# Performance work log

Measured on AMD Instinct MI355X. Metric: run time of the kernel, lower is better.

The kernel has to match this reference:

```python
import jax, jax.numpy as jnp
import numpy as np

DIM = 128
CODEBOOK_SIZE = 1024
DECAY = 0.99
EPSILON = 1e-06


def setup_inputs() -> dict:
    key = jax.random.key(0)
    k1, k2, k3, k4 = jax.random.split(key, 4)
    x = jax.random.normal(k1, (64, 1024, DIM), dtype=jnp.float32)
    embed = jax.random.normal(k2, (CODEBOOK_SIZE, DIM), dtype=jnp.float32)
    # keep all codes above the dead-code threshold (2) so expire_codes_ is a no-op
    cluster_size = jax.random.uniform(k3, (CODEBOOK_SIZE,), dtype=jnp.float32) * 10.0 + 2.0
    embed_avg = jax.random.normal(k4, (CODEBOOK_SIZE, DIM), dtype=jnp.float32)
    return {"x": x, "embed": embed, "cluster_size": cluster_size, "embed_avg": embed_avg}


def reference(x, embed, cluster_size, embed_avg):
    shape = x.shape
    xf = x.reshape(-1, shape[-1])  # [N, D]

    # quantize: squared euclidean distances [N, K] then argmin
    dist = (
        jnp.sum(xf * xf, axis=1, keepdims=True)
        - 2.0 * (xf @ embed.T)
        + jnp.sum(embed * embed, axis=1)[None, :]
    )
    embed_ind_flat = jnp.argmin(dist, axis=-1)  # [N]
    embed_ind = embed_ind_flat.reshape(shape[:-1])

    # dequantize
    quantize = embed[embed_ind]  # [..., D]

    # training EMA updates (one-hot scatter accumulation)
    one_hot_sum = jax.ops.segment_sum(
        jnp.ones_like(embed_ind_flat, dtype=x.dtype), embed_ind_flat,
        num_segments=CODEBOOK_SIZE)
    embed_sum = jax.ops.segment_sum(xf, embed_ind_flat, num_segments=CODEBOOK_SIZE)  # [K, D]

    cluster_size_new = cluster_size * DECAY + one_hot_sum * (1.0 - DECAY)
    embed_avg_new = embed_avg * DECAY + embed_sum * (1.0 - DECAY)

    total = jnp.sum(cluster_size_new)
    smoothed = (cluster_size_new + EPSILON) / (total + EPSILON * CODEBOOK_SIZE) * total
    embed_new = embed_avg_new / smoothed[:, None]

    return quantize, embed_ind, cluster_size_new, embed_avg_new, embed_new
```

## Files before the change

kernel.cpp:

```cpp
#include <hip/hip_runtime.h>
#include <float.h>

#define DIMD   128
#define KCODES 1024
#define NROWS  65536
#define TAU    0.05f
#define SEG_R  8

typedef __attribute__((ext_vector_type(8)))  short short8;
typedef __attribute__((ext_vector_type(16))) float f32x16;

union U8 { uint4 u; short8 s; };

__device__ __forceinline__ unsigned bfr(float f) {
    unsigned u = __float_as_uint(f);
    return (u + 0x7fffu + ((u >> 16) & 1u)) >> 16;
}

__global__ void enorm_kernel(const float* __restrict__ embed, float* __restrict__ enorm) {
    int k = blockIdx.x * blockDim.x + threadIdx.x;
    if (k < KCODES) {
        const float4* e = (const float4*)(embed + (size_t)k * DIMD);
        float s = 0.f;
#pragma unroll
        for (int c = 0; c < DIMD / 4; ++c) {
            float4 v = e[c];
            s += v.x * v.x + v.y * v.y + v.z * v.z + v.w * v.w;
        }
        enorm[k] = s;
    }
}

__global__ __launch_bounds__(256) void preconvert_kernel(
    const float* __restrict__ embed, uint4* __restrict__ ehg, uint4* __restrict__ elg)
{
    int t = blockIdx.x * 256 + threadIdx.x;
    int chunk = t >> 9;
    int s = (t >> 6) & 7;
    int L = t & 63;
    const float* src = embed + ((size_t)(chunk * 32 + (L & 31)) * DIMD) + s * 16 + (L >> 5) * 8;
    float4 a = *(const float4*)src;
    float4 b = *(const float4*)(src + 4);
    float f[8] = {a.x, a.y, a.z, a.w, b.x, b.y, b.z, b.w};
    unsigned hi[8], lo[8];
#pragma unroll
    for (int j = 0; j < 8; ++j) {
        hi[j] = bfr(f[j]);
        float hf = __uint_as_float(hi[j] << 16);
        lo[j] = bfr(f[j] - hf);
    }
    uint4 H, Lw;
    H.x = hi[0] | (hi[1] << 16); H.y = hi[2] | (hi[3] << 16);
    H.z = hi[4] | (hi[5] << 16); H.w = hi[6] | (hi[7] << 16);
    Lw.x = lo[0] | (lo[1] << 16); Lw.y = lo[2] | (lo[3] << 16);
    Lw.z = lo[4] | (lo[5] << 16); Lw.w = lo[6] | (lo[7] << 16);
    ehg[t] = H;
    elg[t] = Lw;
}

__global__ __launch_bounds__(256, 2) void argmin_mfma(
    const float* __restrict__ x, const uint4* __restrict__ ehg, const uint4* __restrict__ elg,
    const float* __restrict__ enorm, int* __restrict__ ind_i, float* __restrict__ ind_f,
    int* __restrict__ wl, int* __restrict__ wl_cnt)
{
    __shared__ uint4 Bs[1024];

    const int tid  = threadIdx.x;
    const int wave = tid >> 6;
    const int lane = tid & 63;
    const int n    = lane & 31;
    const int h    = lane >> 5;
    const int row0 = blockIdx.x * 128;
    const int rowA = row0 + wave * 32 + n;

    uint4 xh[8], xl[8];
    const float* xrow = x + (size_t)rowA * DIMD + h * 8;
#pragma unroll
    for (int s = 0; s < 8; ++s) {
        float4 a = *(const float4*)(xrow + s * 16);
        float4 b = *(const float4*)(xrow + s * 16 + 4);
        float f[8] = {a.x, a.y, a.z, a.w, b.x, b.y, b.z, b.w};
        unsigned hi[8], lo[8];
#pragma unroll
        for (int j = 0; j < 8; ++j) {
            hi[j] = bfr(f[j]);
            float hf = __uint_as_float(hi[j] << 16);
            lo[j] = bfr(f[j] - hf);
        }
        xh[s].x = hi[0] | (hi[1] << 16); xh[s].y = hi[2] | (hi[3] << 16);
        xh[s].z = hi[4] | (hi[5] << 16); xh[s].w = hi[6] | (hi[7] << 16);
        xl[s].x = lo[0] | (lo[1] << 16); xl[s].y = lo[2] | (lo[3] << 16);
        xl[s].z = lo[4] | (lo[5] << 16); xl[s].w = lo[6] | (lo[7] << 16);
    }

    float bestv[16], best2[16];
    int   besti[16];
#pragma unroll
    for (int r = 0; r < 16; ++r) { bestv[r] = FLT_MAX; best2[r] = FLT_MAX; besti[r] = 0; }

    for (int chunk = 0; chunk < KCODES / 32; ++chunk) {
        __syncthreads();
        {
            const uint4* sh = ehg + chunk * 512;
            const uint4* sl = elg + chunk * 512;
#pragma unroll
            for (int i = 0; i < 2; ++i) {
                int idx = tid + i * 256;
                Bs[idx]       = sh[idx];
                Bs[512 + idx] = sl[idx];
            }
        }
        float ee_val = enorm[chunk * 32 + n];
        __syncthreads();

        f32x16 acc;
#pragma unroll
        for (int r = 0; r < 16; ++r) acc[r] = 0.f;

#pragma unroll
        for (int s = 0; s < 8; ++s) {
            U8 ah, al, bh, bl;
            ah.u = xh[s]; al.u = xl[s];
            bh.u = Bs[s * 64 + lane];
            bl.u = Bs[512 + s * 64 + lane];
            acc = __builtin_amdgcn_mfma_f32_32x32x16_bf16(ah.s, bh.s, acc, 0, 0, 0);
            acc = __builtin_amdgcn_mfma_f32_32x32x16_bf16(ah.s, bl.s, acc, 0, 0, 0);
            acc = __builtin_amdgcn_mfma_f32_32x32x16_bf16(al.s, bh.s, acc, 0, 0, 0);
        }

        const int nglob = chunk * 32 + n;
#pragma unroll
        for (int r = 0; r < 16; ++r) {
            float d = fmaf(-2.f, acc[r], ee_val);
            bool c1 = d < bestv[r];
            float t = c1 ? bestv[r] : d;
            best2[r] = fminf(best2[r], t);
            besti[r] = c1 ? nglob : besti[r];
            bestv[r] = fminf(bestv[r], d);
        }
    }

#pragma unroll
    for (int m = 1; m <= 16; m <<= 1) {
#pragma unroll
        for (int r = 0; r < 16; ++r) {
            float ov = __shfl_xor(bestv[r], m, 64);
            float o2 = __shfl_xor(best2[r], m, 64);
            int   oi = __shfl_xor(besti[r], m, 64);
            float hi = fmaxf(bestv[r], ov);
            best2[r] = fminf(fminf(best2[r], o2), hi);
            bool take = (ov < bestv[r]) || (ov == bestv[r] && oi < besti[r]);
            bestv[r] = take ? ov : bestv[r];
            besti[r] = take ? oi : besti[r];
        }
    }

    if (n == 0) {
#pragma unroll
        for (int r = 0; r < 16; ++r) {
            int row = row0 + wave * 32 + (r & 3) + 8 * (r >> 2) + 4 * h;
            ind_i[row] = besti[r];
            ind_f[row] = (float)besti[r];
            if (best2[r] - bestv[r] < TAU) {
                int p = atomicAdd(wl_cnt, 1);
                wl[p] = row;
            }
        }
    }
}

__global__ __launch_bounds__(256) void recheck_kernel(
    const float* __restrict__ x, const float* __restrict__ embed,
    const float* __restrict__ enorm, const int* __restrict__ wl,
    const int* __restrict__ wl_cnt, int* __restrict__ ind_i, float* __restrict__ ind_f)
{
    __shared__ float xs[DIMD];
    __shared__ float rv[256];
    __shared__ int   ri[256];
    const int tid = threadIdx.x;
    const int count = *wl_cnt;

    for (int i = blockIdx.x; i < count; i += gridDim.x) {
        const int row = wl[i];
        __syncthreads();
        if (tid < DIMD) xs[tid] = x[(size_t)row * DIMD + tid];
        __syncthreads();

        const float4* xs4 = (const float4*)xs;
        float xn = 0.f;
#pragma unroll 8
        for (int c = 0; c < 32; ++c) {
            float4 v = xs4[c];
            xn += v.x * v.x + v.y * v.y + v.z * v.z + v.w * v.w;
        }

        float bv = FLT_MAX; int bi = 0;
#pragma unroll
        for (int c = 0; c < 4; ++c) {
            int code = tid * 4 + c;
            const float4* er = (const float4*)(embed + (size_t)code * DIMD);
            float acc = 0.f;
#pragma unroll 8
            for (int kk = 0; kk < 32; ++kk) {
                float4 a = xs4[kk];
                float4 b = er[kk];
                acc += a.x * b.x + a.y * b.y + a.z * b.z + a.w * b.w;
            }
            float d = (xn - 2.0f * acc) + enorm[code];
            if (d < bv) { bv = d; bi = code; }
        }
        rv[tid] = bv; ri[tid] = bi;
        __syncthreads();
        for (int s = 128; s > 0; s >>= 1) {
            if (tid < s) {
                if (rv[tid + s] < rv[tid] || (rv[tid + s] == rv[tid] && ri[tid + s] < ri[tid])) {
                    rv[tid] = rv[tid + s]; ri[tid] = ri[tid + s];
                }
            }
            __syncthreads();
        }
        if (tid == 0) { ind_i[row] = ri[0]; ind_f[row] = (float)ri[0]; }
    }
}

__global__ __launch_bounds__(256) void hist_kernel(
    const int* __restrict__ ind, int* __restrict__ counts)
{
    __shared__ int h[KCODES];
    for (int i = threadIdx.x; i < KCODES; i += 256) h[i] = 0;
    __syncthreads();
    const int base = blockIdx.x * 2048;
    for (int i = threadIdx.x; i < 2048; i += 256) atomicAdd(&h[ind[base + i]], 1);
    __syncthreads();
    for (int i = threadIdx.x; i < KCODES; i += 256) {
        int v = h[i];
        if (v) atomicAdd(&counts[i], v);
    }
}

__global__ __launch_bounds__(1024) void scan_kernel(
    const int* __restrict__ counts, int* __restrict__ cursor)
{
    __shared__ int s[KCODES];
    const int t = threadIdx.x;
    int my = counts[t];
    s[t] = my;
    __syncthreads();
    for (int d = 1; d < KCODES; d <<= 1) {
        int v = (t >= d) ? s[t - d] : 0;
        __syncthreads();
        s[t] += v;
        __syncthreads();
    }
    cursor[t] = s[t] - my;
}

__global__ __launch_bounds__(256) void permgather_kernel(
    const float* __restrict__ embed, const int* __restrict__ ind,
    int* __restrict__ cursor, int* __restrict__ perm, int* __restrict__ codes,
    float* __restrict__ out_q)
{
    const int tid = threadIdx.x;
    const int row = blockIdx.x * 8 + (tid >> 5);
    const int c = tid & 31;
    const int k = ind[row];

    if (c == 0) {
        int pos = atomicAdd(&cursor[k], 1);
        perm[pos] = row;
        codes[pos] = k;
    }
    float4 e = *(const float4*)(embed + (size_t)k * DIMD + c * 4);
    *(float4*)(out_q + (size_t)row * DIMD + c * 4) = e;
}

__global__ __launch_bounds__(256) void segsum_kernel(
    const float* __restrict__ x, const int* __restrict__ perm,
    const int* __restrict__ codes, float* __restrict__ embed_sum)
{
    const int g = (blockIdx.x * 256 + threadIdx.x) >> 5;
    const int c = threadIdx.x & 31;
    const int base = g * SEG_R;

    float4 acc = {0.f, 0.f, 0.f, 0.f};
    int curk = codes[base];
#pragma unroll
    for (int j = 0; j < SEG_R; ++j) {
        int r = perm[base + j];
        int k = codes[base + j];
        float4 v = *(const float4*)(x + (size_t)r * DIMD + c * 4);
        if (k != curk) {
            float* dst = embed_sum + (size_t)curk * DIMD + c * 4;
            atomicAdd(dst + 0, acc.x);
            atomicAdd(dst + 1, acc.y);
            atomicAdd(dst + 2, acc.z);
            atomicAdd(dst + 3, acc.w);
            acc = v;
            curk = k;
        } else {
            acc.x += v.x; acc.y += v.y; acc.z += v.z; acc.w += v.w;
        }
    }
    float* dst = embed_sum + (size_t)curk * DIMD + c * 4;
    atomicAdd(dst + 0, acc.x);
    atomicAdd(dst + 1, acc.y);
    atomicAdd(dst + 2, acc.z);
    atomicAdd(dst + 3, acc.w);
}

__global__ __launch_bounds__(1024) void cluster_kernel(
    const float* __restrict__ cluster_size, const int* __restrict__ counts,
    float* __restrict__ out_cs, float* __restrict__ smoothed)
{
    __shared__ float red[1024];
    const int t = threadIdx.x;
    float cs = cluster_size[t] * 0.99f + (float)counts[t] * 0.01f;
    out_cs[t] = cs;
    red[t] = cs;
    __syncthreads();
    for (int s = 512; s > 0; s >>= 1) {
        if (t < s) red[t] += red[t + s];
        __syncthreads();
    }
    float total = red[0];
    smoothed[t] = (cs + 1e-6f) / (total + 1e-6f * (float)KCODES) * total;
}

__global__ void embed_kernel(
    const float* __restrict__ embed_avg, const float* __restrict__ embed_sum,
    const float* __restrict__ smoothed, float* __restrict__ out_ea,
    float* __restrict__ out_en)
{
    int i = blockIdx.x * blockDim.x + threadIdx.x;
    if (i < KCODES * DIMD) {
        float ea = embed_avg[i] * 0.99f + embed_sum[i] * 0.01f;
        out_ea[i] = ea;
        out_en[i] = ea / smoothed[i >> 7];
    }
}

extern "C" void kernel_launch(void* const* d_in, const int* in_sizes, int n_in,
                              void* d_out, int out_size, void* d_ws, size_t ws_size,
                              hipStream_t stream) {
    const float* x            = (const float*)d_in[0];
    const float* embed        = (const float*)d_in[1];
    const float* cluster_size = (const float*)d_in[2];
    const float* embed_avg    = (const float*)d_in[3];

    float* out     = (float*)d_out;
    float* out_q   = out;
    float* out_ind = out + 8388608;
    float* out_cs  = out + 8454144;
    float* out_ea  = out + 8455168;
    float* out_en  = out + 8586240;

    char* ws = (char*)d_ws;
    int*   ind_i     = (int*)(ws + 0);
    float* enorm     = (float*)(ws + 262144);
    int*   countsI   = (int*)(ws + 266240);
    int*   wl_cnt    = (int*)(ws + 270336);
    int*   cursor    = (int*)(ws + 274432);
    float* smoothed  = (float*)(ws + 278528);
    int*   perm      = (int*)(ws + 286720);
    int*   wl        = (int*)(ws + 548864);
    int*   codes     = (int*)(ws + 548864);
    uint4* ehg       = (uint4*)(ws + 811008);
    uint4* elg       = (uint4*)(ws + 1073152);
    float* embed_sum = (float*)(ws + 811008);

    hipMemsetAsync(countsI, 0, 8192, stream);

    enorm_kernel<<<4, 256, 0, stream>>>(embed, enorm);
    preconvert_kernel<<<64, 256, 0, stream>>>(embed, ehg, elg);
    argmin_mfma<<<NROWS / 128, 256, 0, stream>>>(x, ehg, elg, enorm, ind_i, out_ind, wl, wl_cnt);
    recheck_kernel<<<256, 256, 0, stream>>>(x, embed, enorm, wl, wl_cnt, ind_i, out_ind);
    hist_kernel<<<32, 256, 0, stream>>>(ind_i, countsI);
    scan_kernel<<<1, 1024, 0, stream>>>(countsI, cursor);
    hipMemsetAsync(embed_sum, 0, 524288, stream);
    permgather_kernel<<<NROWS / 8, 256, 0, stream>>>(embed, ind_i, cursor, perm, codes, out_q);
    segsum_kernel<<<(NROWS / SEG_R) * 32 / 256, 256, 0, stream>>>(x, perm, codes, embed_sum);
    cluster_kernel<<<1, 1024, 0, stream>>>(cluster_size, countsI, out_cs, smoothed);
    embed_kernel<<<(KCODES * DIMD + 255) / 256, 256, 0, stream>>>(
        embed_avg, embed_sum, smoothed, out_ea, out_en);
}
```

Baseline: 293.1 us.

## Fuse histogram and dequantize gather into argmin, merge prep and cluster kernels

The enorm and preconvert kernels are merged into one launch. The argmin kernel now stages codebook tiles with direct global-to-LDS loads. It also accumulates code counts with global atomics and writes the quantized output gather itself. The recheck kernel patches counts and out_q when an index changes, and scan and cluster updates are merged into one kernel. This removes several launches and one full pass over the indices, at the cost of about 64K global atomics on 1024 counters and a heavier argmin epilogue.

```diff
diff --git a/kernel.cpp b/kernel.cpp
--- a/kernel.cpp
+++ b/kernel.cpp
@@ -12,14 +12,44 @@
 
 union U8 { uint4 u; short8 s; };
 
+#define GL2LDS(g, l) __builtin_amdgcn_global_load_lds( \
+    (const __attribute__((address_space(1))) void*)(g), \
+    (__attribute__((address_space(3))) void*)(l), 16, 0, 0)
+
 __device__ __forceinline__ unsigned bfr(float f) {
     unsigned u = __float_as_uint(f);
     return (u + 0x7fffu + ((u >> 16) & 1u)) >> 16;
 }
 
-__global__ void enorm_kernel(const float* __restrict__ embed, float* __restrict__ enorm) {
-    int k = blockIdx.x * blockDim.x + threadIdx.x;
-    if (k < KCODES) {
+__global__ __launch_bounds__(256) void pre_kernel(
+    const float* __restrict__ embed, uint4* __restrict__ ehg, uint4* __restrict__ elg,
+    float* __restrict__ enorm)
+{
+    if (blockIdx.x < 64) {
+        int t = blockIdx.x * 256 + threadIdx.x;
+        int chunk = t >> 9;
+        int s = (t >> 6) & 7;
+        int L = t & 63;
+        const float* src = embed + ((size_t)(chunk * 32 + (L & 31)) * DIMD) + s * 16 + (L >> 5) * 8;
+        float4 a = *(const float4*)src;
+        float4 b = *(const float4*)(src + 4);
+        float f[8] = {a.x, a.y, a.z, a.w, b.x, b.y, b.z, b.w};
+        unsigned hi[8], lo[8];
+#pragma unroll
+        for (int j = 0; j < 8; ++j) {
+            hi[j] = bfr(f[j]);
+            float hf = __uint_as_float(hi[j] << 16);
+            lo[j] = bfr(f[j] - hf);
+        }
+        uint4 H, Lw;
+        H.x = hi[0] | (hi[1] << 16); H.y = hi[2] | (hi[3] << 16);
+        H.z = hi[4] | (hi[5] << 16); H.w = hi[6] | (hi[7] << 16);
+        Lw.x = lo[0] | (lo[1] << 16); Lw.y = lo[2] | (lo[3] << 16);
+        Lw.z = lo[4] | (lo[5] << 16); Lw.w = lo[6] | (lo[7] << 16);
+        ehg[t] = H;
+        elg[t] = Lw;
+    } else {
+        int k = (blockIdx.x - 64) * 256 + threadIdx.x;
         const float4* e = (const float4*)(embed + (size_t)k * DIMD);
         float s = 0.f;
 #pragma unroll
@@ -31,39 +61,15 @@
     }
 }
 
-__global__ __launch_bounds__(256) void preconvert_kernel(
-    const float* __restrict__ embed, uint4* __restrict__ ehg, uint4* __restrict__ elg)
-{
-    int t = blockIdx.x * 256 + threadIdx.x;
-    int chunk = t >> 9;
-    int s = (t >> 6) & 7;
-    int L = t & 63;
-    const float* src = embed + ((size_t)(chunk * 32 + (L & 31)) * DIMD) + s * 16 + (L >> 5) * 8;
-    float4 a = *(const float4*)src;
-    float4 b = *(const float4*)(src + 4);
-    float f[8] = {a.x, a.y, a.z, a.w, b.x, b.y, b.z, b.w};
-    unsigned hi[8], lo[8];
-#pragma unroll
-    for (int j = 0; j < 8; ++j) {
-        hi[j] = bfr(f[j]);
-        float hf = __uint_as_float(hi[j] << 16);
-        lo[j] = bfr(f[j] - hf);
-    }
-    uint4 H, Lw;
-    H.x = hi[0] | (hi[1] << 16); H.y = hi[2] | (hi[3] << 16);
-    H.z = hi[4] | (hi[5] << 16); H.w = hi[6] | (hi[7] << 16);
-    Lw.x = lo[0] | (lo[1] << 16); Lw.y = lo[2] | (lo[3] << 16);
-    Lw.z = lo[4] | (lo[5] << 16); Lw.w = lo[6] | (lo[7] << 16);
-    ehg[t] = H;
-    elg[t] = Lw;
-}
-
 __global__ __launch_bounds__(256, 2) void argmin_mfma(
     const float* __restrict__ x, const uint4* __restrict__ ehg, const uint4* __restrict__ elg,
-    const float* __restrict__ enorm, int* __restrict__ ind_i, float* __restrict__ ind_f,
-    int* __restrict__ wl, int* __restrict__ wl_cnt)
+    const float* __restrict__ enorm, const float* __restrict__ embed,
+    int* __restrict__ ind_i, float* __restrict__ ind_f,
+    int* __restrict__ wl, int* __restrict__ wl_cnt,
+    int* __restrict__ counts, float* __restrict__ out_q)
 {
     __shared__ uint4 Bs[1024];
+    __shared__ int s_idx[128];
 
     const int tid  = threadIdx.x;
     const int wave = tid >> 6;
@@ -103,12 +109,11 @@
         {
             const uint4* sh = ehg + chunk * 512;
             const uint4* sl = elg + chunk * 512;
-#pragma unroll
-            for (int i = 0; i < 2; ++i) {
-                int idx = tid + i * 256;
-                Bs[idx]       = sh[idx];
-                Bs[512 + idx] = sl[idx];
-            }
+            const int off = wave * 64 + lane;
+            GL2LDS(sh + off,       &Bs[wave * 64]);
+            GL2LDS(sh + 256 + off, &Bs[256 + wave * 64]);
+            GL2LDS(sl + off,       &Bs[512 + wave * 64]);
+            GL2LDS(sl + 256 + off, &Bs[768 + wave * 64]);
         }
         float ee_val = enorm[chunk * 32 + n];
         __syncthreads();
@@ -158,25 +163,42 @@
     if (n == 0) {
 #pragma unroll
         for (int r = 0; r < 16; ++r) {
-            int row = row0 + wave * 32 + (r & 3) + 8 * (r >> 2) + 4 * h;
+            int local = wave * 32 + (r & 3) + 8 * (r >> 2) + 4 * h;
+            int row = row0 + local;
+            s_idx[local] = besti[r];
             ind_i[row] = besti[r];
             ind_f[row] = (float)besti[r];
+            atomicAdd(&counts[besti[r]], 1);
             if (best2[r] - bestv[r] < TAU) {
                 int p = atomicAdd(wl_cnt, 1);
                 wl[p] = row;
             }
         }
     }
+    __syncthreads();
+
+    const float4* e4 = (const float4*)embed;
+    float4* q4 = (float4*)out_q + (size_t)row0 * 32;
+#pragma unroll
+    for (int j = 0; j < 16; ++j) {
+        int idx4 = tid + 256 * j;
+        int r = idx4 >> 5;
+        int c = idx4 & 31;
+        int k = s_idx[r];
+        q4[r * 32 + c] = e4[(size_t)k * 32 + c];
+    }
 }
 
 __global__ __launch_bounds__(256) void recheck_kernel(
     const float* __restrict__ x, const float* __restrict__ embed,
     const float* __restrict__ enorm, const int* __restrict__ wl,
-    const int* __restrict__ wl_cnt, int* __restrict__ ind_i, float* __restrict__ ind_f)
+    const int* __restrict__ wl_cnt, int* __restrict__ ind_i, float* __restrict__ ind_f,
+    int* __restrict__ counts, float* __restrict__ out_q)
 {
     __shared__ float xs[DIMD];
     __shared__ float rv[256];
     __shared__ int   ri[256];
+    __shared__ int   s_old, s_new;
     const int tid = threadIdx.x;
     const int count = *wl_cnt;
 
@@ -184,6 +206,7 @@
         const int row = wl[i];
         __syncthreads();
         if (tid < DIMD) xs[tid] = x[(size_t)row * DIMD + tid];
+        if (tid == 0) s_old = ind_i[row];
         __syncthreads();
 
         const float4* xs4 = (const float4*)xs;
@@ -219,32 +242,35 @@
             }
             __syncthreads();
         }
-        if (tid == 0) { ind_i[row] = ri[0]; ind_f[row] = (float)ri[0]; }
-    }
-}
-
-__global__ __launch_bounds__(256) void hist_kernel(
-    const int* __restrict__ ind, int* __restrict__ counts)
-{
-    __shared__ int h[KCODES];
-    for (int i = threadIdx.x; i < KCODES; i += 256) h[i] = 0;
-    __syncthreads();
-    const int base = blockIdx.x * 2048;
-    for (int i = threadIdx.x; i < 2048; i += 256) atomicAdd(&h[ind[base + i]], 1);
-    __syncthreads();
-    for (int i = threadIdx.x; i < KCODES; i += 256) {
-        int v = h[i];
-        if (v) atomicAdd(&counts[i], v);
-    }
-}
-
-__global__ __launch_bounds__(1024) void scan_kernel(
-    const int* __restrict__ counts, int* __restrict__ cursor)
-{
-    __shared__ int s[KCODES];
+        if (tid == 0) {
+            s_new = ri[0];
+            if (s_new != s_old) {
+                ind_i[row] = s_new;
+                ind_f[row] = (float)s_new;
+                atomicAdd(&counts[s_old], -1);
+                atomicAdd(&counts[s_new], 1);
+            }
+        }
+        __syncthreads();
+        if (s_new != s_old && tid < 32) {
+            ((float4*)out_q)[(size_t)row * 32 + tid] =
+                ((const float4*)embed)[(size_t)s_new * 32 + tid];
+        }
+    }
+}
+
+__global__ __launch_bounds__(1024) void scan_cluster_kernel(
+    const int* __restrict__ counts, const float* __restrict__ cluster_size,
+    int* __restrict__ cursor, float* __restrict__ out_cs, float* __restrict__ smoothed)
+{
+    __shared__ int   s[KCODES];
+    __shared__ float rf[KCODES];
     const int t = threadIdx.x;
     int my = counts[t];
     s[t] = my;
+    float cs = cluster_size[t] * 0.99f + (float)my * 0.01f;
+    out_cs[t] = cs;
+    rf[t] = cs;
     __syncthreads();
     for (int d = 1; d < KCODES; d <<= 1) {
         int v = (t >= d) ? s[t - d] : 0;
@@ -253,25 +279,23 @@
         __syncthreads();
     }
     cursor[t] = s[t] - my;
-}
-
-__global__ __launch_bounds__(256) void permgather_kernel(
-    const float* __restrict__ embed, const int* __restrict__ ind,
-    int* __restrict__ cursor, int* __restrict__ perm, int* __restrict__ codes,
-    float* __restrict__ out_q)
-{
-    const int tid = threadIdx.x;
-    const int row = blockIdx.x * 8 + (tid >> 5);
-    const int c = tid & 31;
+    for (int st = 512; st > 0; st >>= 1) {
+        if (t < st) rf[t] += rf[t + st];
+        __syncthreads();
+    }
+    float total = rf[0];
+    smoothed[t] = (cs + 1e-6f) / (total + 1e-6f * (float)KCODES) * total;
+}
+
+__global__ __launch_bounds__(256) void permbuild_kernel(
+    const int* __restrict__ ind, int* __restrict__ cursor,
+    int* __restrict__ perm, int* __restrict__ codes)
+{
+    const int row = blockIdx.x * 256 + threadIdx.x;
     const int k = ind[row];
-
-    if (c == 0) {
-        int pos = atomicAdd(&cursor[k], 1);
-        perm[pos] = row;
-        codes[pos] = k;
-    }
-    float4 e = *(const float4*)(embed + (size_t)k * DIMD + c * 4);
-    *(float4*)(out_q + (size_t)row * DIMD + c * 4) = e;
+    int pos = atomicAdd(&cursor[k], 1);
+    perm[pos] = row;
+    codes[pos] = k;
 }
 
 __global__ __launch_bounds__(256) void segsum_kernel(
@@ -308,24 +332,6 @@
     atomicAdd(dst + 3, acc.w);
 }
 
-__global__ __launch_bounds__(1024) void cluster_kernel(
-    const float* __restrict__ cluster_size, const int* __restrict__ counts,
-    float* __restrict__ out_cs, float* __restrict__ smoothed)
-{
-    __shared__ float red[1024];
-    const int t = threadIdx.x;
-    float cs = cluster_size[t] * 0.99f + (float)counts[t] * 0.01f;
-    out_cs[t] = cs;
-    red[t] = cs;
-    __syncthreads();
-    for (int s = 512; s > 0; s >>= 1) {
-        if (t < s) red[t] += red[t + s];
-        __syncthreads();
-    }
-    float total = red[0];
-    smoothed[t] = (cs + 1e-6f) / (total + 1e-6f * (float)KCODES) * total;
-}
-
 __global__ void embed_kernel(
     const float* __restrict__ embed_avg, const float* __restrict__ embed_sum,
     const float* __restrict__ smoothed, float* __restrict__ out_ea,
@@ -370,16 +376,15 @@
 
     hipMemsetAsync(countsI, 0, 8192, stream);
 
-    enorm_kernel<<<4, 256, 0, stream>>>(embed, enorm);
-    preconvert_kernel<<<64, 256, 0, stream>>>(embed, ehg, elg);
-    argmin_mfma<<<NROWS / 128, 256, 0, stream>>>(x, ehg, elg, enorm, ind_i, out_ind, wl, wl_cnt);
-    recheck_kernel<<<256, 256, 0, stream>>>(x, embed, enorm, wl, wl_cnt, ind_i, out_ind);
-    hist_kernel<<<32, 256, 0, stream>>>(ind_i, countsI);
-    scan_kernel<<<1, 1024, 0, stream>>>(countsI, cursor);
+    pre_kernel<<<68, 256, 0, stream>>>(embed, ehg, elg, enorm);
+    argmin_mfma<<<NROWS / 128, 256, 0, stream>>>(
+        x, ehg, elg, enorm, embed, ind_i, out_ind, wl, wl_cnt, countsI, out_q);
+    recheck_kernel<<<256, 256, 0, stream>>>(
+        x, embed, enorm, wl, wl_cnt, ind_i, out_ind, countsI, out_q);
+    scan_cluster_kernel<<<1, 1024, 0, stream>>>(countsI, cluster_size, cursor, out_cs, smoothed);
     hipMemsetAsync(embed_sum, 0, 524288, stream);
-    permgather_kernel<<<NROWS / 8, 256, 0, stream>>>(embed, ind_i, cursor, perm, codes, out_q);
+    permbuild_kernel<<<NROWS / 256, 256, 0, stream>>>(ind_i, cursor, perm, codes);
     segsum_kernel<<<(NROWS / SEG_R) * 32 / 256, 256, 0, stream>>>(x, perm, codes, embed_sum);
-    cluster_kernel<<<1, 1024, 0, stream>>>(cluster_size, countsI, out_cs, smoothed);
     embed_kernel<<<(KCODES * DIMD + 255) / 256, 256, 0, stream>>>(
         embed_avg, embed_sum, smoothed, out_ea, out_en);
 }
```

After: 307.3 us. 4.8% more time.
